# Performance work log

Hardware: AMD Instinct MI355X
Metric: run time of the kernel (lower is better)

The kernel has to match this reference:

```python
import jax, jax.numpy as jnp
import numpy as np

SR = 48000
MAX_DUR = 5.0
N_AUDIO = 480000  # 10 s @ 48 kHz
K_IR = int(SR * MAX_DUR)  # 240000 taps


def setup_inputs() -> dict:
    key = jax.random.key(0)
    k1, k2 = jax.random.split(key)
    audio = jax.random.normal(k1, (N_AUDIO,), dtype=jnp.float32)
    impulse_response = jax.random.normal(k2, (K_IR,), dtype=jnp.float32)
    return {"audio": audio, "impulse_response": impulse_response}


def reference(audio, impulse_response):
    # torch: pad audio with (K-1) zeros, then conv1d (= cross-correlation, no flip)
    K = impulse_response.shape[0]
    a_pad = jnp.concatenate([audio, jnp.zeros((K - 1,), dtype=audio.dtype)])
    # out[t] = sum_k a_pad[t+k] * ir[k], valid correlation -> length N
    out = jnp.correlate(a_pad, impulse_response, mode="valid")
    # trailing peak normalization
    return out / jnp.max(jnp.abs(out))
```

## Files before the change

### kernel.cpp

```cpp
#include <hip/hip_runtime.h>

typedef unsigned int u32;


constexpr int N_AUDIO = 480000;
constexpr int M_FFT   = 1048576;

constexpr size_t OFF_C0   = 0;
constexpr size_t OFF_C1   = (size_t)M_FFT * 8;
constexpr size_t OFF_SLOT = OFF_C1 + (size_t)M_FFT * 8;

#define SW(i) ((i) + ((i) >> 4))
constexpr int LSZ = 1088;

struct F2 { float x, y; };
constexpr double D_PI = 3.14159265358979323846264338327950288;
constexpr double tay_sin(double x) {
    double t = x, s = x, x2 = x * x;
    for (int k = 1; k <= 11; ++k) { t *= -x2 / (double)((2 * k) * (2 * k + 1)); s += t; }
    return s;
}
constexpr double tay_cos(double x) {
    double t = 1.0, s = 1.0, x2 = x * x;
    for (int k = 1; k <= 11; ++k) { t *= -x2 / (double)((2 * k - 1) * (2 * k)); s += t; }
    return s;
}
struct Tab { F2 v[1024]; };
constexpr Tab make_t1() {
    Tab tb{};
    for (int j = 0; j < 1024; ++j) {
        int jj = (j < 512) ? j : j - 1024;
        double a = -2.0 * D_PI * (double)jj / 1024.0;
        tb.v[j] = F2{(float)tay_cos(a), (float)tay_sin(a)};
    }
    return tb;
}
constexpr Tab make_t2() {
    Tab tb{};
    for (int j = 0; j < 1024; ++j) {
        double a = -2.0 * D_PI * (double)j / 1048576.0;
        tb.v[j] = F2{(float)tay_cos(a), (float)tay_sin(a)};
    }
    return tb;
}
__device__ constexpr Tab ROM_T1 = make_t1();
__device__ constexpr Tab ROM_T2 = make_t2();

__device__ __forceinline__ float2 ldrom(const Tab& tb, int i) {
    F2 f = tb.v[i];
    return make_float2(f.x, f.y);
}
__device__ __forceinline__ float2 cmul(float2 a, float2 b) {
    return make_float2(a.x * b.x - a.y * b.y, a.x * b.y + a.y * b.x);
}
__device__ __forceinline__ void stage_tabs(float2* lt1, float2* lt2, int t) {
    #pragma unroll
    for (int q = 0; q < 4; ++q) {
        int i = t + 256 * q;
        lt1[i] = ldrom(ROM_T1, i);
        lt2[i] = ldrom(ROM_T2, i);
    }
}

__device__ __forceinline__ void fft1024_r4(float2 (*A0)[LSZ], float2 (*B0)[LSZ],
                                           const float2* lt1, int t) {
    float2 (*A)[LSZ] = A0;
    float2 (*B)[LSZ] = B0;
    #pragma unroll
    for (int s = 0; s < 5; ++s) {
        const int L  = 1 << (2 * s);
        const int k  = t & (L - 1);
        const int p0 = 4 * t - 3 * k;
        const float2 w  = lt1[k << (9 - 2 * s)];
        const float2 w2 = lt1[k << (8 - 2 * s)];
        #pragma unroll
        for (int j = 0; j < 2; ++j) {
            float2 x0 = A[j][SW(t)];
            float2 x2 = A[j][SW(t + 256)];
            float2 x1 = A[j][SW(t + 512)];
            float2 x3 = A[j][SW(t + 768)];
            float2 wx1 = cmul(w, x1), wx3 = cmul(w, x3);
            float2 u0 = make_float2(x0.x + wx1.x, x0.y + wx1.y);
            float2 u1 = make_float2(x0.x - wx1.x, x0.y - wx1.y);
            float2 u2 = make_float2(x2.x + wx3.x, x2.y + wx3.y);
            float2 u3 = make_float2(x2.x - wx3.x, x2.y - wx3.y);
            float2 a2 = cmul(w2, u2);
            float2 a3 = cmul(w2, u3);
            B[j][SW(p0)]         = make_float2(u0.x + a2.x, u0.y + a2.y);
            B[j][SW(p0 + L)]     = make_float2(u1.x + a3.y, u1.y - a3.x);
            B[j][SW(p0 + 2*L)]   = make_float2(u0.x - a2.x, u0.y - a2.y);
            B[j][SW(p0 + 3*L)]   = make_float2(u1.x - a3.y, u1.y + a3.x);
        }
        __syncthreads();
        float2 (*tmp)[LSZ] = A; A = B; B = tmp;
    }
}

__global__ __launch_bounds__(256) void kA(const float* __restrict__ a,
                                          const float* __restrict__ b,
                                          float2* __restrict__ outb,
                                          u32* __restrict__ slot) {
    __shared__ float2 buf0[2][LSZ], buf1[2][LSZ], lt1[1024], lt2[1024];
    const int t  = threadIdx.x;
    const int r0 = blockIdx.x * 2;
    if (blockIdx.x == 0 && t == 0) *slot = 0u;
    stage_tabs(lt1, lt2, t);
    #pragma unroll
    for (int q = 0; q < 4; ++q) {
        int c = t + 256 * q;
        int base = c * 1024 + r0;
        float2 av = make_float2(0.f, 0.f), bv = make_float2(0.f, 0.f);
        if (c < 468 || (c == 468 && r0 < 768)) av = *(const float2*)(a + base);
        if (c < 234 || (c == 234 && r0 < 384)) bv = *(const float2*)(b + base);
        buf0[0][SW(c)] = make_float2(av.x, bv.x);
        buf0[1][SW(c)] = make_float2(av.y, bv.y);
    }
    __syncthreads();
    fft1024_r4(buf0, buf1, lt1, t);
    #pragma unroll
    for (int q = 0; q < 4; ++q) {
        int k1 = t + 256 * q;
        #pragma unroll
        for (int j = 0; j < 2; ++j) {
            int e = (r0 + j) * k1;
            float2 w = cmul(lt1[e >> 10], lt2[e & 1023]);
            outb[(r0 + j) * 1024 + k1] = cmul(w, buf1[j][SW(k1)]);
        }
    }
}

__global__ __launch_bounds__(256) void kBC(const float2* __restrict__ in,
                                           float2* __restrict__ outb) {
    __shared__ float2 buf0[2][LSZ], buf1[2][LSZ], lt1[1024], lt2[1024];
    const int t = threadIdx.x;
    const int bidx = blockIdx.x;
    const int cA = (bidx == 0) ? 0   : bidx;
    const int cB = (bidx == 0) ? 512 : 1024 - bidx;
    stage_tabs(lt1, lt2, t);
    #pragma unroll
    for (int q = 0; q < 4; ++q) {
        int r = t + 256 * q;
        buf0[0][SW(r)] = in[r * 1024 + cA];
        buf0[1][SW(r)] = in[r * 1024 + cB];
    }
    __syncthreads();
    fft1024_r4(buf0, buf1, lt1, t);
    const float invM = 1.0f / 1048576.0f;
    #pragma unroll
    for (int q = 0; q < 4; ++q) {
        int k2 = t + 256 * q;
        #pragma unroll
        for (int j = 0; j < 2; ++j) {
            float2 z1 = buf1[j][SW(k2)];
            float2 z2;
            if (bidx == 0) z2 = (j == 0) ? buf1[0][SW((1024 - k2) & 1023)]
                                         : buf1[1][SW(1023 - k2)];
            else           z2 = buf1[j ^ 1][SW(1023 - k2)];
            float2 Af  = make_float2(0.5f * (z1.x + z2.x), 0.5f * (z1.y - z2.y));
            float2 cBf = make_float2(0.5f * (z1.y + z2.y), 0.5f * (z1.x - z2.x));
            float2 S   = cmul(Af, cBf);
            buf0[j][SW(k2)] = make_float2(S.x * invM, -S.y * invM);
        }
    }
    __syncthreads();
    fft1024_r4(buf0, buf1, lt1, t);
    #pragma unroll
    for (int q = 0; q < 4; ++q) {
        int k1 = t + 256 * q;
        #pragma unroll
        for (int j = 0; j < 2; ++j) {
            int cc = (j == 0) ? cA : cB;
            int e  = cc * k1;
            float2 w = cmul(lt1[e >> 10], lt2[e & 1023]);
            outb[cc * 1024 + k1] = cmul(w, buf1[j][SW(k1)]);
        }
    }
}

__global__ __launch_bounds__(256) void kD(const float2* __restrict__ in,
                                          float* __restrict__ rawT,
                                          u32* __restrict__ slot) {
    __shared__ float2 buf0[2][LSZ], buf1[2][LSZ], lt1[1024];
    __shared__ float wmax[4];
    const int t  = threadIdx.x;
    const int c0 = blockIdx.x * 2;
    #pragma unroll
    for (int q = 0; q < 4; ++q) { int i = t + 256 * q; lt1[i] = ldrom(ROM_T1, i); }
    #pragma unroll
    for (int q = 0; q < 4; ++q) {
        int r = t + 256 * q;
        float4 v = *(const float4*)(in + (size_t)r * 1024 + c0);
        buf0[0][SW(r)] = make_float2(v.x, v.y);
        buf0[1][SW(r)] = make_float2(v.z, v.w);
    }
    __syncthreads();
    fft1024_r4(buf0, buf1, lt1, t);
    float m = 0.0f;
    #pragma unroll
    for (int q = 0; q < 4; ++q) {
        int k2 = t + 256 * q;
        #pragma unroll
        for (int j = 0; j < 2; ++j) {
            int ot = c0 + j + (k2 << 10);
            if (ot < N_AUDIO) {
                float v = buf1[j][SW(k2)].x;
                rawT[(c0 + j) * 512 + k2] = v;
                m = fmaxf(m, fabsf(v));
            }
        }
    }
    for (int off = 32; off > 0; off >>= 1) m = fmaxf(m, __shfl_down(m, off, 64));
    if ((t & 63) == 0) wmax[t >> 6] = m;
    __syncthreads();
    if (t == 0) {
        float bm = fmaxf(fmaxf(wmax[0], wmax[1]), fmaxf(wmax[2], wmax[3]));
        atomicMax(slot, __float_as_uint(bm));
    }
}

__global__ __launch_bounds__(256) void kE(const float* __restrict__ rawT,
                                          const u32* __restrict__ slot,
                                          float* __restrict__ out) {
    __shared__ float tile[64][65];
    const int t  = threadIdx.x;
    const int c0 = (blockIdx.x & 15) * 64;
    const int k0 = (blockIdx.x >> 4) * 64;
    const int cl = t >> 2, ch = (t & 3) * 16;
    #pragma unroll
    for (int i = 0; i < 4; ++i) {
        float4 v = *(const float4*)(rawT + (size_t)(c0 + cl) * 512 + k0 + ch + i * 4);
        tile[cl][ch + i * 4 + 0] = v.x;
        tile[cl][ch + i * 4 + 1] = v.y;
        tile[cl][ch + i * 4 + 2] = v.z;
        tile[cl][ch + i * 4 + 3] = v.w;
    }
    __syncthreads();
    const float inv = 1.0f / __uint_as_float(*slot);
    const int cw = t & 63, w = t >> 6;
    #pragma unroll
    for (int q = 0; q < 16; ++q) {
        int kk = q * 4 + w;
        int o = (k0 + kk) * 1024 + c0 + cw;
        if (o < N_AUDIO) out[o] = tile[cw][kk] * inv;
    }
}

extern "C" void kernel_launch(void* const* d_in, const int* in_sizes, int n_in,
                              void* d_out, int out_size, void* d_ws, size_t ws_size,
                              hipStream_t stream) {
    const float* audio = (const float*)d_in[0];
    const float* ir    = (const float*)d_in[1];
    float* out = (float*)d_out;

    char* ws = (char*)d_ws;
    float2* cb0 = (float2*)(ws + OFF_C0);
    float2* cb1 = (float2*)(ws + OFF_C1);
    u32*    slot = (u32*)(ws + OFF_SLOT);

    kA<<<512, 256, 0, stream>>>(audio, ir, cb1, slot);
    kBC<<<512, 256, 0, stream>>>(cb1, cb0);
    kD<<<512, 256, 0, stream>>>(cb0, (float*)cb1, slot);
    kE<<<128, 256, 0, stream>>>((const float*)cb1, slot, out);
}
```

Baseline: 104.4 us.

## Use half-length complex inverse FFT for real output via even/odd packing

The inverse transform now exploits the real-valued output. The spectrum is folded into a half-size complex spectrum with even/odd twiddle post-processing, so the inverse path runs a 512-point column FFT in kBC and half as many 1024-point row FFTs in kD (256 blocks instead of 512). kE is rewritten to unpack interleaved real pairs and write float2 outputs. This roughly halves the inverse FFT work and its global traffic, at the cost of extra pre-twiddle arithmetic and a new transpose layout.

```diff
diff --git a/kernel.cpp b/kernel.cpp
--- a/kernel.cpp
+++ b/kernel.cpp
@@ -96,6 +96,50 @@
     }
 }
 
+__device__ __forceinline__ void fft512_r4(float2 (*A0)[LSZ], float2 (*B0)[LSZ],
+                                          const float2* lt1, int t) {
+    float2 (*A)[LSZ] = A0;
+    float2 (*B)[LSZ] = B0;
+    const int j  = t >> 7;
+    const int tt = t & 127;
+    #pragma unroll
+    for (int s = 0; s < 4; ++s) {
+        const int L  = 1 << (2 * s);
+        const int k  = tt & (L - 1);
+        const int p0 = 4 * tt - 3 * k;
+        const float2 w  = lt1[k << (9 - 2 * s)];
+        const float2 w2 = lt1[k << (8 - 2 * s)];
+        float2 x0 = A[j][SW(tt)];
+        float2 x2 = A[j][SW(tt + 128)];
+        float2 x1 = A[j][SW(tt + 256)];
+        float2 x3 = A[j][SW(tt + 384)];
+        float2 wx1 = cmul(w, x1), wx3 = cmul(w, x3);
+        float2 u0 = make_float2(x0.x + wx1.x, x0.y + wx1.y);
+        float2 u1 = make_float2(x0.x - wx1.x, x0.y - wx1.y);
+        float2 u2 = make_float2(x2.x + wx3.x, x2.y + wx3.y);
+        float2 u3 = make_float2(x2.x - wx3.x, x2.y - wx3.y);
+        float2 a2 = cmul(w2, u2);
+        float2 a3 = cmul(w2, u3);
+        B[j][SW(p0)]       = make_float2(u0.x + a2.x, u0.y + a2.y);
+        B[j][SW(p0 + L)]   = make_float2(u1.x + a3.y, u1.y - a3.x);
+        B[j][SW(p0 + 2*L)] = make_float2(u0.x - a2.x, u0.y - a2.y);
+        B[j][SW(p0 + 3*L)] = make_float2(u1.x - a3.y, u1.y + a3.x);
+        __syncthreads();
+        float2 (*tmp)[LSZ] = A; A = B; B = tmp;
+    }
+    #pragma unroll
+    for (int h = 0; h < 2; ++h) {
+        int i = tt + 128 * h;
+        float2 x0 = A[j][SW(i)];
+        float2 x1 = A[j][SW(i + 256)];
+        float2 w  = lt1[i << 1];
+        float2 wx = cmul(w, x1);
+        B[j][SW(i)]       = make_float2(x0.x + wx.x, x0.y + wx.y);
+        B[j][SW(i + 256)] = make_float2(x0.x - wx.x, x0.y - wx.y);
+    }
+    __syncthreads();
+}
+
 __global__ __launch_bounds__(256) void kA(const float* __restrict__ a,
                                           const float* __restrict__ b,
                                           float2* __restrict__ outb,
@@ -130,7 +174,7 @@
 }
 
 __global__ __launch_bounds__(256) void kBC(const float2* __restrict__ in,
-                                           float2* __restrict__ outb) {
+                                           float2* __restrict__ gbuf) {
     __shared__ float2 buf0[2][LSZ], buf1[2][LSZ], lt1[1024], lt2[1024];
     const int t = threadIdx.x;
     const int bidx = blockIdx.x;
@@ -145,7 +189,6 @@
     }
     __syncthreads();
     fft1024_r4(buf0, buf1, lt1, t);
-    const float invM = 1.0f / 1048576.0f;
     #pragma unroll
     for (int q = 0; q < 4; ++q) {
         int k2 = t + 256 * q;
@@ -158,40 +201,60 @@
             else           z2 = buf1[j ^ 1][SW(1023 - k2)];
             float2 Af  = make_float2(0.5f * (z1.x + z2.x), 0.5f * (z1.y - z2.y));
             float2 cBf = make_float2(0.5f * (z1.y + z2.y), 0.5f * (z1.x - z2.x));
-            float2 S   = cmul(Af, cBf);
-            buf0[j][SW(k2)] = make_float2(S.x * invM, -S.y * invM);
-        }
-    }
-    __syncthreads();
-    fft1024_r4(buf0, buf1, lt1, t);
-    #pragma unroll
-    for (int q = 0; q < 4; ++q) {
-        int k1 = t + 256 * q;
-        #pragma unroll
-        for (int j = 0; j < 2; ++j) {
-            int cc = (j == 0) ? cA : cB;
-            int e  = cc * k1;
-            float2 w = cmul(lt1[e >> 10], lt2[e & 1023]);
-            outb[cc * 1024 + k1] = cmul(w, buf1[j][SW(k1)]);
-        }
-    }
-}
-
-__global__ __launch_bounds__(256) void kD(const float2* __restrict__ in,
-                                          float* __restrict__ rawT,
+            buf0[j][SW(k2)] = cmul(Af, cBf);
+        }
+    }
+    __syncthreads();
+    const float invN2 = 1.0f / 524288.0f;
+    #pragma unroll
+    for (int j = 0; j < 2; ++j) {
+        const int bcol = (j == 0) ? cA : cB;
+        const float2 wb = lt2[bcol];
+        #pragma unroll
+        for (int h = 0; h < 2; ++h) {
+            int k2v = t + 256 * h;
+            float2 z1 = buf0[j][SW(k2v)];
+            int jr, p2;
+            if (bidx == 0) { jr = j; p2 = (j == 0) ? (512 - k2v) : (511 - k2v); }
+            else           { jr = j ^ 1; p2 = 511 - k2v; }
+            float2 z2c = buf0[jr][SW(p2)];
+            z2c.y = -z2c.y;
+            float2 A2 = make_float2(0.5f * (z1.x + z2c.x), 0.5f * (z1.y + z2c.y));
+            float2 D2 = make_float2(0.5f * (z1.x - z2c.x), 0.5f * (z1.y - z2c.y));
+            float2 cw = cmul(lt1[k2v], wb);
+            float2 iB = cmul(make_float2(cw.y, cw.x), D2);
+            float2 Z  = make_float2(A2.x + iB.x, A2.y + iB.y);
+            buf1[j][SW(k2v)] = make_float2(Z.x * invN2, -Z.y * invN2);
+        }
+    }
+    __syncthreads();
+    fft512_r4(buf1, buf0, lt1, t);
+    const int jc = t >> 7, tt = t & 127;
+    const int bcol = (jc == 0) ? cA : cB;
+    #pragma unroll
+    for (int u = 0; u < 4; ++u) {
+        int k1 = tt + 128 * u;
+        int e2 = 2 * bcol * k1;
+        float2 w = cmul(lt1[e2 >> 10], lt2[e2 & 1023]);
+        gbuf[bcol * 512 + k1] = cmul(w, buf0[jc][SW(k1)]);
+    }
+}
+
+__global__ __launch_bounds__(256) void kD(const float2* __restrict__ gbuf,
+                                          float2* __restrict__ rawT2,
                                           u32* __restrict__ slot) {
     __shared__ float2 buf0[2][LSZ], buf1[2][LSZ], lt1[1024];
     __shared__ float wmax[4];
-    const int t  = threadIdx.x;
-    const int c0 = blockIdx.x * 2;
+    const int t = threadIdx.x;
+    const int qb = blockIdx.x;
     #pragma unroll
     for (int q = 0; q < 4; ++q) { int i = t + 256 * q; lt1[i] = ldrom(ROM_T1, i); }
     #pragma unroll
     for (int q = 0; q < 4; ++q) {
-        int r = t + 256 * q;
-        float4 v = *(const float4*)(in + (size_t)r * 1024 + c0);
-        buf0[0][SW(r)] = make_float2(v.x, v.y);
-        buf0[1][SW(r)] = make_float2(v.z, v.w);
+        int b = t + 256 * q;
+        float4 v = *(const float4*)(gbuf + (size_t)b * 512 + 2 * qb);
+        buf0[0][SW(b)] = make_float2(v.x, v.y);
+        buf0[1][SW(b)] = make_float2(v.z, v.w);
     }
     __syncthreads();
     fft1024_r4(buf0, buf1, lt1, t);
@@ -201,11 +264,12 @@
         int k2 = t + 256 * q;
         #pragma unroll
         for (int j = 0; j < 2; ++j) {
-            int ot = c0 + j + (k2 << 10);
-            if (ot < N_AUDIO) {
-                float v = buf1[j][SW(k2)].x;
-                rawT[(c0 + j) * 512 + k2] = v;
-                m = fmaxf(m, fabsf(v));
+            int k1 = 2 * qb + j;
+            int to = 2 * k1 + 1024 * k2;
+            if (to < N_AUDIO) {
+                float2 v = buf1[j][SW(k2)];
+                rawT2[k1 * 1024 + k2] = make_float2(v.x, -v.y);
+                m = fmaxf(m, fmaxf(fabsf(v.x), fabsf(v.y)));
             }
         }
     }
@@ -218,30 +282,30 @@
     }
 }
 
-__global__ __launch_bounds__(256) void kE(const float* __restrict__ rawT,
+__global__ __launch_bounds__(256) void kE(const float2* __restrict__ rawT2,
                                           const u32* __restrict__ slot,
                                           float* __restrict__ out) {
-    __shared__ float tile[64][65];
+    __shared__ float2 tile[64][65];
     const int t  = threadIdx.x;
-    const int c0 = (blockIdx.x & 15) * 64;
-    const int k0 = (blockIdx.x >> 4) * 64;
-    const int cl = t >> 2, ch = (t & 3) * 16;
-    #pragma unroll
-    for (int i = 0; i < 4; ++i) {
-        float4 v = *(const float4*)(rawT + (size_t)(c0 + cl) * 512 + k0 + ch + i * 4);
-        tile[cl][ch + i * 4 + 0] = v.x;
-        tile[cl][ch + i * 4 + 1] = v.y;
-        tile[cl][ch + i * 4 + 2] = v.z;
-        tile[cl][ch + i * 4 + 3] = v.w;
+    const int K0 = (blockIdx.x & 7) * 64;
+    const int Q0 = (blockIdx.x >> 3) * 64;
+    #pragma unroll
+    for (int i = 0; i < 16; ++i) {
+        int idx = t + 256 * i;
+        int row = idx >> 6, col = idx & 63;
+        tile[col][row] = rawT2[(size_t)(K0 + row) * 1024 + Q0 + col];
     }
     __syncthreads();
     const float inv = 1.0f / __uint_as_float(*slot);
-    const int cw = t & 63, w = t >> 6;
-    #pragma unroll
-    for (int q = 0; q < 16; ++q) {
-        int kk = q * 4 + w;
-        int o = (k0 + kk) * 1024 + c0 + cw;
-        if (o < N_AUDIO) out[o] = tile[cw][kk] * inv;
+    #pragma unroll
+    for (int i = 0; i < 16; ++i) {
+        int idx = t + 256 * i;
+        int cc = idx >> 6, rr = idx & 63;
+        int o = (Q0 + cc) * 1024 + 2 * (K0 + rr);
+        if (o < N_AUDIO) {
+            float2 v = tile[cc][rr];
+            *(float2*)(out + o) = make_float2(v.x * inv, v.y * inv);
+        }
     }
 }
 
@@ -259,6 +323,6 @@
 
     kA<<<512, 256, 0, stream>>>(audio, ir, cb1, slot);
     kBC<<<512, 256, 0, stream>>>(cb1, cb0);
-    kD<<<512, 256, 0, stream>>>(cb0, (float*)cb1, slot);
-    kE<<<128, 256, 0, stream>>>((const float*)cb1, slot, out);
-}
+    kD<<<256, 256, 0, stream>>>(cb0, cb1, slot);
+    kE<<<128, 256, 0, stream>>>((const float2*)cb1, slot, out);
+}
```

New measurement: 98.42 us. 1.06x faster.
